# Performance work log

Hardware: AMD Instinct MI355X
Metric: run time of the kernel (lower is better)

## Reference

```python
import jax, jax.numpy as jnp
import numpy as np

B, T, S, H = 8, 512, 512, 128


def setup_inputs() -> dict:
    key = jax.random.key(0)
    ks = jax.random.split(key, 8)
    query = jax.random.normal(ks[0], (B, T, H), dtype=jnp.float32)
    encoder_outputs = jax.random.normal(ks[1], (B, S, H), dtype=jnp.float32)
    src_lengths = jax.random.randint(ks[2], (B,), 1, S + 1)
    src_lengths = src_lengths.at[0].set(S)  # torch mask width == lengths.max() must equal S
    scale = 1.0 / np.sqrt(H)
    W_h = jax.random.normal(ks[3], (H, H), dtype=jnp.float32) * scale
    W_s = jax.random.normal(ks[4], (H, H), dtype=jnp.float32) * scale
    v = jax.random.normal(ks[5], (H,), dtype=jnp.float32) * scale
    W_out_w = jax.random.normal(ks[6], (H, 2 * H), dtype=jnp.float32) * (1.0 / np.sqrt(2 * H))
    W_out_b = jax.random.normal(ks[7], (H,), dtype=jnp.float32) * 0.01
    return {"query": query, "encoder_outputs": encoder_outputs,
            "src_lengths": src_lengths, "W_h": W_h, "W_s": W_s, "v": v,
            "W_out_w": W_out_w, "W_out_b": W_out_b}


def reference(query, encoder_outputs, src_lengths, W_h, W_s, v, W_out_w, W_out_b):
    # query: (B,T,H); encoder_outputs: (B,S,H)
    S_ = encoder_outputs.shape[1]
    WS = jnp.einsum('bth,oh->bto', query, W_s)            # (B,T,H)
    WH = jnp.einsum('bsh,oh->bso', encoder_outputs, W_h)  # (B,S,H)
    # additive scores: v^T tanh(W_s s_t + W_h h_i)  -> (B,T,S)
    scores = jnp.einsum('btsh,h->bts', jnp.tanh(WS[:, :, None, :] + WH[:, None, :, :]), v)
    mask = jnp.arange(S_) < src_lengths[:, None]          # (B,S)
    # faithful quirk: original zeroes (not -inf) masked scores before softmax
    scores = jnp.where(mask[:, None, :], scores, 0.0)
    attn = jax.nn.softmax(scores, axis=-1)                # (B,T,S)
    ct = jnp.einsum('bts,bsh->bth', attn, encoder_outputs)
    concat = jnp.concatenate([ct, query], axis=-1)        # (B,T,2H)
    return jnp.tanh(jnp.einsum('btc,oc->bto', concat, W_out_w) + W_out_b)
```

## Files before the change

### kernel.cpp

```cpp
#include <hip/hip_runtime.h>
#include <hip/hip_fp16.h>

#define NB 8
#define NT 512
#define NS 512
#define NH 128
#define C2LOG2E 2.8853900817779268f

__device__ __forceinline__ float fast_exp2(float x) { return __builtin_amdgcn_exp2f(x); }
__device__ __forceinline__ float fast_rcp(float x)  { return __builtin_amdgcn_rcpf(x); }
__device__ __forceinline__ float fast_tanh(float x) {
  float e = fast_exp2(x * C2LOG2E);
  return 1.0f - 2.0f * fast_rcp(e + 1.0f);
}

__device__ __forceinline__ float dot4(float4 a, float4 b) {
  return (a.x * b.x + a.y * b.y) + (a.z * b.z + a.w * b.w);
}

__device__ __forceinline__ float2 quad_acc2(float4 e, float4 vv,
                                            float2 F0, float2 F1,
                                            float2 F2, float2 F3, float2 acc) {
  float P0x = fmaf(e.x, F0.x, 1.f), P0y = fmaf(e.x, F0.y, 1.f);
  float P1x = fmaf(e.y, F1.x, 1.f), P1y = fmaf(e.y, F1.y, 1.f);
  float P2x = fmaf(e.z, F2.x, 1.f), P2y = fmaf(e.z, F2.y, 1.f);
  float P3x = fmaf(e.w, F3.x, 1.f), P3y = fmaf(e.w, F3.y, 1.f);
  float d01x = P0x * P1x, d01y = P0y * P1y;
  float d23x = P2x * P3x, d23y = P2y * P3y;
  float n01x = fmaf(vv.x, P1x, vv.y * P0x);
  float n01y = fmaf(vv.x, P1y, vv.y * P0y);
  float n23x = fmaf(vv.z, P3x, vv.w * P2x);
  float n23y = fmaf(vv.z, P3y, vv.w * P2y);
  float numx = fmaf(n01x, d23x, n23x * d01x);
  float numy = fmaf(n01y, d23y, n23y * d01y);
  acc.x = fmaf(numx, fast_rcp(d01x * d23x), acc.x);
  acc.y = fmaf(numy, fast_rcp(d01y * d23y), acc.y);
  return acc;
}

__global__ __launch_bounds__(256) void bah_proj_kernel(
    const float* __restrict__ query, const float* __restrict__ enc,
    const float* __restrict__ W_s, const float* __restrict__ W_h,
    const float* __restrict__ Wout, const float* __restrict__ Woutb,
    float* __restrict__ EWS, __half* __restrict__ EWHT,
    __half* __restrict__ ENCW, float* __restrict__ QW2) {
  __shared__ __align__(16) float lds_w[64 * 132];
  __shared__ __align__(16) float lds_x[64 * 132];
  const int set = blockIdx.x >> 7;
  const int blk = blockIdx.x & 127;
  const int rb = blk >> 1, ch = blk & 1;
  const int r0 = rb * 64, c0 = ch * 64;
  const int tid = threadIdx.x;
  const float* in = (set == 1 || set == 2) ? enc : query;
  const float* Wb; int wst;
  if (set == 0)      { Wb = W_s;        wst = 128; }
  else if (set == 1) { Wb = W_h;        wst = 128; }
  else if (set == 2) { Wb = Wout;       wst = 256; }
  else               { Wb = Wout + 128; wst = 256; }
  for (int i = tid; i < 2048; i += 256) {
    int r = i >> 5, c4 = i & 31;
    *(float4*)(lds_w + r * 132 + c4 * 4) =
        *(const float4*)(Wb + (c0 + r) * wst + c4 * 4);
  }
  for (int i = tid; i < 2048; i += 256) {
    int r = i >> 5, c4 = i & 31;
    *(float4*)(lds_x + r * 132 + c4 * 4) =
        *(const float4*)(in + (r0 + r) * NH + c4 * 4);
  }
  __syncthreads();
  const int colg = tid & 15;
  const int rowg = tid >> 4;
  float acc[4][4] = {{0,0,0,0},{0,0,0,0},{0,0,0,0},{0,0,0,0}};
  for (int k4 = 0; k4 < 32; ++k4) {
    float4 xa[4], wb[4];
    #pragma unroll
    for (int i = 0; i < 4; ++i)
      xa[i] = *(const float4*)(lds_x + (rowg * 4 + i) * 132 + k4 * 4);
    #pragma unroll
    for (int m = 0; m < 4; ++m)
      wb[m] = *(const float4*)(lds_w + (colg + 16 * m) * 132 + k4 * 4);
    #pragma unroll
    for (int i = 0; i < 4; ++i)
      #pragma unroll
      for (int m = 0; m < 4; ++m)
        acc[i][m] += dot4(xa[i], wb[m]);
  }
  if (set == 0) {
    #pragma unroll
    for (int i = 0; i < 4; ++i)
      #pragma unroll
      for (int m = 0; m < 4; ++m)
        EWS[(r0 + rowg * 4 + i) * NH + c0 + colg + 16 * m] =
            fast_exp2(C2LOG2E * acc[i][m]);
  } else if (set == 1) {
    __syncthreads();
    #pragma unroll
    for (int i = 0; i < 4; ++i)
      #pragma unroll
      for (int m = 0; m < 4; ++m)
        lds_x[(colg + 16 * m) * 68 + rowg * 4 + i] =
            fminf(fast_exp2(C2LOG2E * acc[i][m]), 60000.f);
    __syncthreads();
    const int b = r0 >> 9, sl0 = r0 & 511;
    const int sc = tid & 15, hb = tid >> 4;
    #pragma unroll
    for (int g = 0; g < 4; ++g) {
      int h = hb + 16 * g;
      float4 f = *(const float4*)(lds_x + h * 68 + sc * 4);
      __half2 p01 = __floats2half2_rn(f.x, f.y);
      __half2 p23 = __floats2half2_rn(f.z, f.w);
      __half2* dst = (__half2*)(EWHT + (size_t)b * NH * NS +
                                (c0 + h) * NS + sl0 + sc * 4);
      dst[0] = p01; dst[1] = p23;
    }
  } else if (set == 2) {
    #pragma unroll
    for (int i = 0; i < 4; ++i)
      #pragma unroll
      for (int m = 0; m < 4; ++m)
        ENCW[(r0 + rowg * 4 + i) * NH + c0 + colg + 16 * m] =
            __float2half_rn(acc[i][m]);
  } else {
    #pragma unroll
    for (int i = 0; i < 4; ++i)
      #pragma unroll
      for (int m = 0; m < 4; ++m) {
        int c = c0 + colg + 16 * m;
        QW2[(r0 + rowg * 4 + i) * NH + c] = acc[i][m] + Woutb[c];
      }
  }
}

__global__ __launch_bounds__(256) void bah_mega_kernel(
    const float* __restrict__ EWS, const __half* __restrict__ EWHT,
    const float* __restrict__ v, const __half* __restrict__ ENCW,
    const float* __restrict__ QW2, const int* __restrict__ src_len,
    float* __restrict__ out) {
  __shared__ __align__(16) float smem[4784];
  float* s_v   = smem;
  float* s_et  = smem + 128;
  float* s_aT  = smem + 656;
  float* s_sc  = smem + 2704;
  float* s_red = smem + 4768;

  const int tid = threadIdx.x;
  const int bb = blockIdx.x >> 7;
  const int t0 = (blockIdx.x & 127) * 4;
  const int len = src_len[bb];

  if (tid < 32) *(float4*)(s_v + tid * 4) = *(const float4*)(v + tid * 4);
  if (tid < 128) {
    int r = tid >> 5, c4 = tid & 31;
    *(float4*)(s_et + r * 132 + c4 * 4) =
        *(const float4*)(EWS + (bb * NT + t0 + r) * NH + c4 * 4);
  }
  __syncthreads();

  float V0;
  {
    float2 vv = *(const float2*)(s_v + (tid & 63) * 2);
    V0 = vv.x + vv.y;
    #pragma unroll
    for (int msk = 1; msk <= 32; msk <<= 1)
      V0 += __shfl_xor(V0, msk, 64);
  }

  const int sbase = tid * 2;
  float2 acc2[4];
  #pragma unroll
  for (int i = 0; i < 4; ++i) { acc2[i].x = 0.f; acc2[i].y = 0.f; }
  const int wave_s0 = (tid & ~63) * 2;
  if (wave_s0 < len) {
    const __half2* fb = (const __half2*)EWHT + (size_t)bb * NH * 256 + tid;
    for (int ho = 0; ho < 16; ++ho) {
      const __half2* fh = fb + ho * 8 * 256;
      float2 F0 = __half22float2(fh[0 * 256]);
      float2 F1 = __half22float2(fh[1 * 256]);
      float2 F2 = __half22float2(fh[2 * 256]);
      float2 F3 = __half22float2(fh[3 * 256]);
      float2 F4 = __half22float2(fh[4 * 256]);
      float2 F5 = __half22float2(fh[5 * 256]);
      float2 F6 = __half22float2(fh[6 * 256]);
      float2 F7 = __half22float2(fh[7 * 256]);
      float4 va = *(const float4*)(s_v + ho * 8);
      float4 vb = *(const float4*)(s_v + ho * 8 + 4);
      #pragma unroll
      for (int tt = 0; tt < 4; ++tt) {
        float4 e0 = *(const float4*)(s_et + tt * 132 + ho * 8);
        float4 e1 = *(const float4*)(s_et + tt * 132 + ho * 8 + 4);
        acc2[tt] = quad_acc2(e0, va, F0, F1, F2, F3, acc2[tt]);
        acc2[tt] = quad_acc2(e1, vb, F4, F5, F6, F7, acc2[tt]);
      }
    }
  }
  #pragma unroll
  for (int tt = 0; tt < 4; ++tt) {
    float2 r;
    r.x = (sbase + 0 < len) ? fmaf(-2.f, acc2[tt].x, V0) : 0.f;
    r.y = (sbase + 1 < len) ? fmaf(-2.f, acc2[tt].y, V0) : 0.f;
    *(float2*)(s_sc + tt * 516 + sbase) = r;
  }
  __syncthreads();

  const int t = tid & 3;
  const int c = tid >> 2;
  const int wv = tid >> 6;
  float pv[8];
  float mx = -3.4e38f;
  #pragma unroll
  for (int k = 0; k < 8; ++k) {
    pv[k] = s_sc[t * 516 + c + 64 * k];
    mx = fmaxf(mx, pv[k]);
  }
  #pragma unroll
  for (int msk = 4; msk <= 32; msk <<= 1)
    mx = fmaxf(mx, __shfl_xor(mx, msk, 64));
  if ((tid & 63) < 4) s_red[wv * 4 + t] = mx;
  __syncthreads();
  #pragma unroll
  for (int j = 0; j < 4; ++j) mx = fmaxf(mx, s_red[j * 4 + t]);
  __syncthreads();
  float sum = 0.f;
  #pragma unroll
  for (int k = 0; k < 8; ++k) {
    pv[k] = fast_exp2((pv[k] - mx) * 1.4426950408889634f);
    sum += pv[k];
  }
  #pragma unroll
  for (int msk = 4; msk <= 32; msk <<= 1)
    sum += __shfl_xor(sum, msk, 64);
  if ((tid & 63) < 4) s_red[wv * 4 + t] = sum;
  __syncthreads();
  sum = 0.f;
  #pragma unroll
  for (int j = 0; j < 4; ++j) sum += s_red[j * 4 + t];
  const float rd = fast_rcp(sum);
  #pragma unroll
  for (int k = 0; k < 8; ++k)
    s_aT[(c + 64 * k) * 4 + t] = pv[k] * rd;
  __syncthreads();

  const int hg = tid & 31, sg = tid >> 5;
  float4 a8[4] = {{0,0,0,0},{0,0,0,0},{0,0,0,0},{0,0,0,0}};
  const __half2* eb = (const __half2*)ENCW + (size_t)bb * NS * 64 + hg * 2;
  for (int k = 0; k < 64; ++k) {
    int s = sg * 64 + k;
    uint2 raw = *(const uint2*)(eb + s * 64);
    float2 f0 = __half22float2(*(const __half2*)&raw.x);
    float2 f1 = __half22float2(*(const __half2*)&raw.y);
    float4 e = {f0.x, f0.y, f1.x, f1.y};
    float4 w = *(const float4*)(s_aT + s * 4);
    a8[0].x += w.x*e.x; a8[0].y += w.x*e.y; a8[0].z += w.x*e.z; a8[0].w += w.x*e.w;
    a8[1].x += w.y*e.x; a8[1].y += w.y*e.y; a8[1].z += w.y*e.z; a8[1].w += w.y*e.w;
    a8[2].x += w.z*e.x; a8[2].y += w.z*e.y; a8[2].z += w.z*e.z; a8[2].w += w.z*e.w;
    a8[3].x += w.w*e.x; a8[3].y += w.w*e.y; a8[3].z += w.w*e.z; a8[3].w += w.w*e.w;
  }
  #pragma unroll
  for (int i = 0; i < 4; ++i) {
    a8[i].x += __shfl_xor(a8[i].x, 32, 64);
    a8[i].y += __shfl_xor(a8[i].y, 32, 64);
    a8[i].z += __shfl_xor(a8[i].z, 32, 64);
    a8[i].w += __shfl_xor(a8[i].w, 32, 64);
  }
  float* lred = s_sc;
  if ((tid & 63) < 32) {
    #pragma unroll
    for (int i = 0; i < 4; ++i)
      *(float4*)(lred + wv * 512 + i * 128 + hg * 4) = a8[i];
  }
  __syncthreads();
  {
    int tt = tid >> 6, h2 = tid & 63;
    float2 o = {0.f, 0.f};
    #pragma unroll
    for (int j = 0; j < 4; ++j) {
      float2 p = *(const float2*)(lred + j * 512 + tt * 128 + h2 * 2);
      o.x += p.x; o.y += p.y;
    }
    const int row = bb * NT + t0 + tt;
    float2 q2 = *(const float2*)(QW2 + row * NH + h2 * 2);
    float2 r;
    r.x = fast_tanh(o.x + q2.x);
    r.y = fast_tanh(o.y + q2.y);
    *(float2*)(out + row * NH + h2 * 2) = r;
  }
}

extern "C" void kernel_launch(void* const* d_in, const int* in_sizes, int n_in,
                              void* d_out, int out_size, void* d_ws, size_t ws_size,
                              hipStream_t stream) {
  const float* query = (const float*)d_in[0];
  const float* enc   = (const float*)d_in[1];
  const int*   slen  = (const int*)d_in[2];
  const float* W_h   = (const float*)d_in[3];
  const float* W_s   = (const float*)d_in[4];
  const float* v     = (const float*)d_in[5];
  const float* Woutw = (const float*)d_in[6];
  const float* Woutb = (const float*)d_in[7];
  float* out = (float*)d_out;

  float* ws = (float*)d_ws;
  float*  EWS  = ws;
  float*  QW2  = ws + 524288;
  __half* EWHT = (__half*)(ws + 1048576);
  __half* ENCW = (__half*)(ws + 1310720);

  bah_proj_kernel<<<512, 256, 0, stream>>>(query, enc, W_s, W_h, Woutw,
                                           Woutb, EWS, EWHT, ENCW, QW2);
  bah_mega_kernel<<<1024, 256, 0, stream>>>(EWS, EWHT, v, ENCW, QW2, slen, out);
}
```

Before: 120.1 us.

## Halve queries per block in attention kernel and stage ENCW stores through LDS

The main attention kernel now handles 2 query rows per block instead of 4 and launches twice as many blocks. This shrinks the per-block shared-memory and register footprint and adds a launch bound hinting 8 blocks per CU, aiming for higher occupancy. The trade-off is that each block re-reads the EWHT and ENCW tiles for half as many queries, which doubles that global/L2 traffic. Separately, the projection kernel's ENCW fp16 output is staged through LDS so each thread writes 16-byte vector stores instead of scattered 2-byte stores.

```diff
diff --git a/kernel.cpp b/kernel.cpp
--- a/kernel.cpp
+++ b/kernel.cpp
@@ -114,12 +114,22 @@
       dst[0] = p01; dst[1] = p23;
     }
   } else if (set == 2) {
+    __syncthreads();
     #pragma unroll
     for (int i = 0; i < 4; ++i)
       #pragma unroll
       for (int m = 0; m < 4; ++m)
-        ENCW[(r0 + rowg * 4 + i) * NH + c0 + colg + 16 * m] =
-            __float2half_rn(acc[i][m]);
+        lds_w[(rowg * 4 + i) * 68 + colg + 16 * m] = acc[i][m];
+    __syncthreads();
+    const int rr = tid >> 2, cb = (tid & 3) * 16;
+    const float* src = lds_w + rr * 68 + cb;
+    __half2 h[8];
+    #pragma unroll
+    for (int q = 0; q < 8; ++q)
+      h[q] = __floats2half2_rn(src[2 * q], src[2 * q + 1]);
+    uint4* dst = (uint4*)(ENCW + (size_t)(r0 + rr) * NH + c0 + cb);
+    dst[0] = ((uint4*)h)[0];
+    dst[1] = ((uint4*)h)[1];
   } else {
     #pragma unroll
     for (int i = 0; i < 4; ++i)
@@ -131,25 +141,25 @@
   }
 }
 
-__global__ __launch_bounds__(256) void bah_mega_kernel(
+__global__ __launch_bounds__(256, 8) void bah_mega_kernel(
     const float* __restrict__ EWS, const __half* __restrict__ EWHT,
     const float* __restrict__ v, const __half* __restrict__ ENCW,
     const float* __restrict__ QW2, const int* __restrict__ src_len,
     float* __restrict__ out) {
-  __shared__ __align__(16) float smem[4784];
+  __shared__ __align__(16) float smem[2456];
   float* s_v   = smem;
   float* s_et  = smem + 128;
-  float* s_aT  = smem + 656;
-  float* s_sc  = smem + 2704;
-  float* s_red = smem + 4768;
+  float* s_aT  = smem + 392;
+  float* s_sc  = smem + 1416;
+  float* s_red = smem + 2448;
 
   const int tid = threadIdx.x;
-  const int bb = blockIdx.x >> 7;
-  const int t0 = (blockIdx.x & 127) * 4;
+  const int bb = blockIdx.x >> 8;
+  const int t0 = (blockIdx.x & 255) * 2;
   const int len = src_len[bb];
 
   if (tid < 32) *(float4*)(s_v + tid * 4) = *(const float4*)(v + tid * 4);
-  if (tid < 128) {
+  if (tid < 64) {
     int r = tid >> 5, c4 = tid & 31;
     *(float4*)(s_et + r * 132 + c4 * 4) =
         *(const float4*)(EWS + (bb * NT + t0 + r) * NH + c4 * 4);
@@ -166,9 +176,8 @@
   }
 
   const int sbase = tid * 2;
-  float2 acc2[4];
-  #pragma unroll
-  for (int i = 0; i < 4; ++i) { acc2[i].x = 0.f; acc2[i].y = 0.f; }
+  float2 acc2[2];
+  acc2[0].x = 0.f; acc2[0].y = 0.f; acc2[1].x = 0.f; acc2[1].y = 0.f;
   const int wave_s0 = (tid & ~63) * 2;
   if (wave_s0 < len) {
     const __half2* fb = (const __half2*)EWHT + (size_t)bb * NH * 256 + tid;
@@ -185,7 +194,7 @@
       float4 va = *(const float4*)(s_v + ho * 8);
       float4 vb = *(const float4*)(s_v + ho * 8 + 4);
       #pragma unroll
-      for (int tt = 0; tt < 4; ++tt) {
+      for (int tt = 0; tt < 2; ++tt) {
         float4 e0 = *(const float4*)(s_et + tt * 132 + ho * 8);
         float4 e1 = *(const float4*)(s_et + tt * 132 + ho * 8 + 4);
         acc2[tt] = quad_acc2(e0, va, F0, F1, F2, F3, acc2[tt]);
@@ -194,7 +203,7 @@
     }
   }
   #pragma unroll
-  for (int tt = 0; tt < 4; ++tt) {
+  for (int tt = 0; tt < 2; ++tt) {
     float2 r;
     r.x = (sbase + 0 < len) ? fmaf(-2.f, acc2[tt].x, V0) : 0.f;
     r.y = (sbase + 1 < len) ? fmaf(-2.f, acc2[tt].y, V0) : 0.f;
@@ -202,87 +211,78 @@
   }
   __syncthreads();
 
-  const int t = tid & 3;
-  const int c = tid >> 2;
+  const int t = tid & 1;
+  const int c = tid >> 1;
   const int wv = tid >> 6;
-  float pv[8];
+  float pv[4];
   float mx = -3.4e38f;
   #pragma unroll
-  for (int k = 0; k < 8; ++k) {
-    pv[k] = s_sc[t * 516 + c + 64 * k];
+  for (int k = 0; k < 4; ++k) {
+    pv[k] = s_sc[t * 516 + c + 128 * k];
     mx = fmaxf(mx, pv[k]);
   }
   #pragma unroll
-  for (int msk = 4; msk <= 32; msk <<= 1)
+  for (int msk = 2; msk <= 32; msk <<= 1)
     mx = fmaxf(mx, __shfl_xor(mx, msk, 64));
-  if ((tid & 63) < 4) s_red[wv * 4 + t] = mx;
-  __syncthreads();
-  #pragma unroll
-  for (int j = 0; j < 4; ++j) mx = fmaxf(mx, s_red[j * 4 + t]);
+  if ((tid & 63) < 2) s_red[wv * 2 + t] = mx;
+  __syncthreads();
+  #pragma unroll
+  for (int j = 0; j < 4; ++j) mx = fmaxf(mx, s_red[j * 2 + t]);
   __syncthreads();
   float sum = 0.f;
   #pragma unroll
-  for (int k = 0; k < 8; ++k) {
+  for (int k = 0; k < 4; ++k) {
     pv[k] = fast_exp2((pv[k] - mx) * 1.4426950408889634f);
     sum += pv[k];
   }
   #pragma unroll
-  for (int msk = 4; msk <= 32; msk <<= 1)
+  for (int msk = 2; msk <= 32; msk <<= 1)
     sum += __shfl_xor(sum, msk, 64);
-  if ((tid & 63) < 4) s_red[wv * 4 + t] = sum;
+  if ((tid & 63) < 2) s_red[wv * 2 + t] = sum;
   __syncthreads();
   sum = 0.f;
   #pragma unroll
-  for (int j = 0; j < 4; ++j) sum += s_red[j * 4 + t];
+  for (int j = 0; j < 4; ++j) sum += s_red[j * 2 + t];
   const float rd = fast_rcp(sum);
   #pragma unroll
-  for (int k = 0; k < 8; ++k)
-    s_aT[(c + 64 * k) * 4 + t] = pv[k] * rd;
+  for (int k = 0; k < 4; ++k)
+    s_aT[(c + 128 * k) * 2 + t] = pv[k] * rd;
   __syncthreads();
 
   const int hg = tid & 31, sg = tid >> 5;
-  float4 a8[4] = {{0,0,0,0},{0,0,0,0},{0,0,0,0},{0,0,0,0}};
+  float4 a0 = {0,0,0,0}, a1 = {0,0,0,0};
   const __half2* eb = (const __half2*)ENCW + (size_t)bb * NS * 64 + hg * 2;
   for (int k = 0; k < 64; ++k) {
     int s = sg * 64 + k;
     uint2 raw = *(const uint2*)(eb + s * 64);
     float2 f0 = __half22float2(*(const __half2*)&raw.x);
     float2 f1 = __half22float2(*(const __half2*)&raw.y);
-    float4 e = {f0.x, f0.y, f1.x, f1.y};
-    float4 w = *(const float4*)(s_aT + s * 4);
-    a8[0].x += w.x*e.x; a8[0].y += w.x*e.y; a8[0].z += w.x*e.z; a8[0].w += w.x*e.w;
-    a8[1].x += w.y*e.x; a8[1].y += w.y*e.y; a8[1].z += w.y*e.z; a8[1].w += w.y*e.w;
-    a8[2].x += w.z*e.x; a8[2].y += w.z*e.y; a8[2].z += w.z*e.z; a8[2].w += w.z*e.w;
-    a8[3].x += w.w*e.x; a8[3].y += w.w*e.y; a8[3].z += w.w*e.z; a8[3].w += w.w*e.w;
-  }
-  #pragma unroll
-  for (int i = 0; i < 4; ++i) {
-    a8[i].x += __shfl_xor(a8[i].x, 32, 64);
-    a8[i].y += __shfl_xor(a8[i].y, 32, 64);
-    a8[i].z += __shfl_xor(a8[i].z, 32, 64);
-    a8[i].w += __shfl_xor(a8[i].w, 32, 64);
-  }
+    float2 w = *(const float2*)(s_aT + s * 2);
+    a0.x += w.x*f0.x; a0.y += w.x*f0.y; a0.z += w.x*f1.x; a0.w += w.x*f1.y;
+    a1.x += w.y*f0.x; a1.y += w.y*f0.y; a1.z += w.y*f1.x; a1.w += w.y*f1.y;
+  }
+  a0.x += __shfl_xor(a0.x, 32, 64);
+  a0.y += __shfl_xor(a0.y, 32, 64);
+  a0.z += __shfl_xor(a0.z, 32, 64);
+  a0.w += __shfl_xor(a0.w, 32, 64);
+  a1.x += __shfl_xor(a1.x, 32, 64);
+  a1.y += __shfl_xor(a1.y, 32, 64);
+  a1.z += __shfl_xor(a1.z, 32, 64);
+  a1.w += __shfl_xor(a1.w, 32, 64);
   float* lred = s_sc;
   if ((tid & 63) < 32) {
-    #pragma unroll
-    for (int i = 0; i < 4; ++i)
-      *(float4*)(lred + wv * 512 + i * 128 + hg * 4) = a8[i];
+    *(float4*)(lred + wv * 256 + hg * 4) = a0;
+    *(float4*)(lred + wv * 256 + 128 + hg * 4) = a1;
   }
   __syncthreads();
   {
-    int tt = tid >> 6, h2 = tid & 63;
-    float2 o = {0.f, 0.f};
-    #pragma unroll
-    for (int j = 0; j < 4; ++j) {
-      float2 p = *(const float2*)(lred + j * 512 + tt * 128 + h2 * 2);
-      o.x += p.x; o.y += p.y;
-    }
+    int tt = tid >> 7, hh = tid & 127;
+    float o = 0.f;
+    #pragma unroll
+    for (int j = 0; j < 4; ++j)
+      o += lred[j * 256 + tt * 128 + hh];
     const int row = bb * NT + t0 + tt;
-    float2 q2 = *(const float2*)(QW2 + row * NH + h2 * 2);
-    float2 r;
-    r.x = fast_tanh(o.x + q2.x);
-    r.y = fast_tanh(o.y + q2.y);
-    *(float2*)(out + row * NH + h2 * 2) = r;
+    out[row * NH + hh] = fast_tanh(o + QW2[row * NH + hh]);
   }
 }
 
@@ -307,5 +307,5 @@
 
   bah_proj_kernel<<<512, 256, 0, stream>>>(query, enc, W_s, W_h, Woutw,
                                            Woutb, EWS, EWHT, ENCW, QW2);
-  bah_mega_kernel<<<1024, 256, 0, stream>>>(EWS, EWHT, v, ENCW, QW2, slen, out);
-}
+  bah_mega_kernel<<<2048, 256, 0, stream>>>(EWS, EWHT, v, ENCW, QW2, slen, out);
+}
```

New measurement: 119.9 us. About the same (-0.1%).

## Split mega kernel into score and context kernels via half-precision attention buffer

Applied to the files above, without the earlier changes.

Splits the fused score+context kernel in two. The score kernel writes transposed softmax weights as fp16 to a workspace buffer. A separate context kernel with 512 threads then handles 8 query rows per block, so each ENCW element loaded is reused across more rows. The ENCW store in the projection kernel is also staged through LDS so it can be written with wide vector stores. The trade is an extra launch, an extra global round trip for the attention matrix, and fp16 rounding of the attention weights.

```diff
diff --git a/kernel.cpp b/kernel.cpp
--- a/kernel.cpp
+++ b/kernel.cpp
@@ -114,12 +114,22 @@
       dst[0] = p01; dst[1] = p23;
     }
   } else if (set == 2) {
+    __syncthreads();
     #pragma unroll
     for (int i = 0; i < 4; ++i)
       #pragma unroll
       for (int m = 0; m < 4; ++m)
-        ENCW[(r0 + rowg * 4 + i) * NH + c0 + colg + 16 * m] =
-            __float2half_rn(acc[i][m]);
+        lds_w[(rowg * 4 + i) * 68 + colg + 16 * m] = acc[i][m];
+    __syncthreads();
+    const int rr = tid >> 2, cb = (tid & 3) * 16;
+    const float* src = lds_w + rr * 68 + cb;
+    __half2 h[8];
+    #pragma unroll
+    for (int q = 0; q < 8; ++q)
+      h[q] = __floats2half2_rn(src[2 * q], src[2 * q + 1]);
+    uint4* dst = (uint4*)(ENCW + (size_t)(r0 + rr) * NH + c0 + cb);
+    dst[0] = ((uint4*)h)[0];
+    dst[1] = ((uint4*)h)[1];
   } else {
     #pragma unroll
     for (int i = 0; i < 4; ++i)
@@ -131,17 +141,15 @@
   }
 }
 
-__global__ __launch_bounds__(256) void bah_mega_kernel(
+__global__ __launch_bounds__(256) void bah_score_kernel(
     const float* __restrict__ EWS, const __half* __restrict__ EWHT,
-    const float* __restrict__ v, const __half* __restrict__ ENCW,
-    const float* __restrict__ QW2, const int* __restrict__ src_len,
-    float* __restrict__ out) {
-  __shared__ __align__(16) float smem[4784];
+    const float* __restrict__ v, const int* __restrict__ src_len,
+    __half* __restrict__ aT) {
+  __shared__ __align__(16) float smem[2736];
   float* s_v   = smem;
   float* s_et  = smem + 128;
-  float* s_aT  = smem + 656;
-  float* s_sc  = smem + 2704;
-  float* s_red = smem + 4768;
+  float* s_sc  = smem + 656;
+  float* s_red = smem + 2720;
 
   const int tid = threadIdx.x;
   const int bb = blockIdx.x >> 7;
@@ -235,54 +243,74 @@
   #pragma unroll
   for (int j = 0; j < 4; ++j) sum += s_red[j * 4 + t];
   const float rd = fast_rcp(sum);
+  __half* ab = aT + (size_t)bb * NS * NT + t0 + t;
   #pragma unroll
   for (int k = 0; k < 8; ++k)
-    s_aT[(c + 64 * k) * 4 + t] = pv[k] * rd;
-  __syncthreads();
-
+    ab[(size_t)(c + 64 * k) * NT] = __float2half_rn(pv[k] * rd);
+}
+
+__global__ __launch_bounds__(512) void bah_ct_kernel(
+    const __half* __restrict__ aT, const __half* __restrict__ ENCW,
+    const float* __restrict__ QW2, float* __restrict__ out) {
+  __shared__ __align__(16) float lred[8192];
+  const int tid = threadIdx.x;
+  const int bb = blockIdx.x >> 6;
+  const int t0 = (blockIdx.x & 63) * 8;
   const int hg = tid & 31, sg = tid >> 5;
-  float4 a8[4] = {{0,0,0,0},{0,0,0,0},{0,0,0,0},{0,0,0,0}};
+  const int wv = tid >> 6;
+
+  float4 a8[8] = {{0,0,0,0},{0,0,0,0},{0,0,0,0},{0,0,0,0},
+                  {0,0,0,0},{0,0,0,0},{0,0,0,0},{0,0,0,0}};
   const __half2* eb = (const __half2*)ENCW + (size_t)bb * NS * 64 + hg * 2;
-  for (int k = 0; k < 64; ++k) {
-    int s = sg * 64 + k;
-    uint2 raw = *(const uint2*)(eb + s * 64);
+  const __half* wb = aT + (size_t)bb * NS * NT + t0;
+  for (int k = 0; k < 32; ++k) {
+    int s = sg * 32 + k;
+    uint2 raw = *(const uint2*)(eb + (size_t)s * 64);
     float2 f0 = __half22float2(*(const __half2*)&raw.x);
     float2 f1 = __half22float2(*(const __half2*)&raw.y);
     float4 e = {f0.x, f0.y, f1.x, f1.y};
-    float4 w = *(const float4*)(s_aT + s * 4);
-    a8[0].x += w.x*e.x; a8[0].y += w.x*e.y; a8[0].z += w.x*e.z; a8[0].w += w.x*e.w;
-    a8[1].x += w.y*e.x; a8[1].y += w.y*e.y; a8[1].z += w.y*e.z; a8[1].w += w.y*e.w;
-    a8[2].x += w.z*e.x; a8[2].y += w.z*e.y; a8[2].z += w.z*e.z; a8[2].w += w.z*e.w;
-    a8[3].x += w.w*e.x; a8[3].y += w.w*e.y; a8[3].z += w.w*e.z; a8[3].w += w.w*e.w;
-  }
-  #pragma unroll
-  for (int i = 0; i < 4; ++i) {
+    uint4 wraw = *(const uint4*)(wb + (size_t)s * NT);
+    const __half2* wh = (const __half2*)&wraw;
+    float2 w01 = __half22float2(wh[0]);
+    float2 w23 = __half22float2(wh[1]);
+    float2 w45 = __half22float2(wh[2]);
+    float2 w67 = __half22float2(wh[3]);
+    float w[8] = {w01.x, w01.y, w23.x, w23.y, w45.x, w45.y, w67.x, w67.y};
+    #pragma unroll
+    for (int i = 0; i < 8; ++i) {
+      a8[i].x += w[i] * e.x; a8[i].y += w[i] * e.y;
+      a8[i].z += w[i] * e.z; a8[i].w += w[i] * e.w;
+    }
+  }
+  #pragma unroll
+  for (int i = 0; i < 8; ++i) {
     a8[i].x += __shfl_xor(a8[i].x, 32, 64);
     a8[i].y += __shfl_xor(a8[i].y, 32, 64);
     a8[i].z += __shfl_xor(a8[i].z, 32, 64);
     a8[i].w += __shfl_xor(a8[i].w, 32, 64);
   }
-  float* lred = s_sc;
   if ((tid & 63) < 32) {
     #pragma unroll
-    for (int i = 0; i < 4; ++i)
-      *(float4*)(lred + wv * 512 + i * 128 + hg * 4) = a8[i];
-  }
-  __syncthreads();
-  {
-    int tt = tid >> 6, h2 = tid & 63;
-    float2 o = {0.f, 0.f};
-    #pragma unroll
-    for (int j = 0; j < 4; ++j) {
-      float2 p = *(const float2*)(lred + j * 512 + tt * 128 + h2 * 2);
-      o.x += p.x; o.y += p.y;
+    for (int i = 0; i < 8; ++i)
+      *(float4*)(lred + wv * 1024 + i * 128 + hg * 4) = a8[i];
+  }
+  __syncthreads();
+  if (tid < 256) {
+    int tt = tid >> 5, hh = tid & 31;
+    float4 o = {0.f, 0.f, 0.f, 0.f};
+    #pragma unroll
+    for (int j = 0; j < 8; ++j) {
+      float4 p = *(const float4*)(lred + j * 1024 + tt * 128 + hh * 4);
+      o.x += p.x; o.y += p.y; o.z += p.z; o.w += p.w;
     }
     const int row = bb * NT + t0 + tt;
-    float2 q2 = *(const float2*)(QW2 + row * NH + h2 * 2);
-    float2 r;
-    r.x = fast_tanh(o.x + q2.x);
-    r.y = fast_tanh(o.y + q2.y);
-    *(float2*)(out + row * NH + h2 * 2) = r;
+    float4 q4 = *(const float4*)(QW2 + row * NH + hh * 4);
+    float4 r;
+    r.x = fast_tanh(o.x + q4.x);
+    r.y = fast_tanh(o.y + q4.y);
+    r.z = fast_tanh(o.z + q4.z);
+    r.w = fast_tanh(o.w + q4.w);
+    *(float4*)(out + row * NH + hh * 4) = r;
   }
 }
 
@@ -304,8 +332,10 @@
   float*  QW2  = ws + 524288;
   __half* EWHT = (__half*)(ws + 1048576);
   __half* ENCW = (__half*)(ws + 1310720);
+  __half* aT   = (__half*)(ws + 1572864);
 
   bah_proj_kernel<<<512, 256, 0, stream>>>(query, enc, W_s, W_h, Woutw,
                                            Woutb, EWS, EWHT, ENCW, QW2);
-  bah_mega_kernel<<<1024, 256, 0, stream>>>(EWS, EWHT, v, ENCW, QW2, slen, out);
-}
+  bah_score_kernel<<<1024, 256, 0, stream>>>(EWS, EWHT, v, slen, aT);
+  bah_ct_kernel<<<512, 512, 0, stream>>>(aT, ENCW, QW2, out);
+}
```

Result: slower. 123.4 us (+2.8%).

## Prefetch global loads one iteration ahead and coalesce ENCW stores via LDS

Applied to the files above, without the earlier changes.

The score loop now loads the next group of eight EWHT half2 values into registers while computing on the current group, and the context loop prefetches the next ENCW row the same way. Both are meant to hide global-load latency behind FMA work. The ENCW write in the projection kernel is staged through LDS so each thread stores two 16-byte vectors instead of scattered 2-byte halves. This adds register pressure and extra barriers, which may reduce occupancy.

```diff
diff --git a/kernel.cpp b/kernel.cpp
--- a/kernel.cpp
+++ b/kernel.cpp
@@ -114,12 +114,22 @@
       dst[0] = p01; dst[1] = p23;
     }
   } else if (set == 2) {
+    __syncthreads();
     #pragma unroll
     for (int i = 0; i < 4; ++i)
       #pragma unroll
       for (int m = 0; m < 4; ++m)
-        ENCW[(r0 + rowg * 4 + i) * NH + c0 + colg + 16 * m] =
-            __float2half_rn(acc[i][m]);
+        lds_w[(rowg * 4 + i) * 68 + colg + 16 * m] = acc[i][m];
+    __syncthreads();
+    const int rr = tid >> 2, cb = (tid & 3) * 16;
+    const float* src = lds_w + rr * 68 + cb;
+    __half2 h[8];
+    #pragma unroll
+    for (int q = 0; q < 8; ++q)
+      h[q] = __floats2half2_rn(src[2 * q], src[2 * q + 1]);
+    uint4* dst = (uint4*)(ENCW + (size_t)(r0 + rr) * NH + c0 + cb);
+    dst[0] = ((uint4*)h)[0];
+    dst[1] = ((uint4*)h)[1];
   } else {
     #pragma unroll
     for (int i = 0; i < 4; ++i)
@@ -172,16 +182,24 @@
   const int wave_s0 = (tid & ~63) * 2;
   if (wave_s0 < len) {
     const __half2* fb = (const __half2*)EWHT + (size_t)bb * NH * 256 + tid;
+    __half2 F[8];
+    #pragma unroll
+    for (int j = 0; j < 8; ++j) F[j] = fb[j * 256];
     for (int ho = 0; ho < 16; ++ho) {
-      const __half2* fh = fb + ho * 8 * 256;
-      float2 F0 = __half22float2(fh[0 * 256]);
-      float2 F1 = __half22float2(fh[1 * 256]);
-      float2 F2 = __half22float2(fh[2 * 256]);
-      float2 F3 = __half22float2(fh[3 * 256]);
-      float2 F4 = __half22float2(fh[4 * 256]);
-      float2 F5 = __half22float2(fh[5 * 256]);
-      float2 F6 = __half22float2(fh[6 * 256]);
-      float2 F7 = __half22float2(fh[7 * 256]);
+      __half2 Fn[8];
+      if (ho < 15) {
+        const __half2* fh = fb + (ho + 1) * 8 * 256;
+        #pragma unroll
+        for (int j = 0; j < 8; ++j) Fn[j] = fh[j * 256];
+      }
+      float2 F0 = __half22float2(F[0]);
+      float2 F1 = __half22float2(F[1]);
+      float2 F2 = __half22float2(F[2]);
+      float2 F3 = __half22float2(F[3]);
+      float2 F4 = __half22float2(F[4]);
+      float2 F5 = __half22float2(F[5]);
+      float2 F6 = __half22float2(F[6]);
+      float2 F7 = __half22float2(F[7]);
       float4 va = *(const float4*)(s_v + ho * 8);
       float4 vb = *(const float4*)(s_v + ho * 8 + 4);
       #pragma unroll
@@ -191,6 +209,8 @@
         acc2[tt] = quad_acc2(e0, va, F0, F1, F2, F3, acc2[tt]);
         acc2[tt] = quad_acc2(e1, vb, F4, F5, F6, F7, acc2[tt]);
       }
+      #pragma unroll
+      for (int j = 0; j < 8; ++j) F[j] = Fn[j];
     }
   }
   #pragma unroll
@@ -243,9 +263,11 @@
   const int hg = tid & 31, sg = tid >> 5;
   float4 a8[4] = {{0,0,0,0},{0,0,0,0},{0,0,0,0},{0,0,0,0}};
   const __half2* eb = (const __half2*)ENCW + (size_t)bb * NS * 64 + hg * 2;
+  uint2 raw = *(const uint2*)(eb + (size_t)(sg * 64) * 64);
   for (int k = 0; k < 64; ++k) {
     int s = sg * 64 + k;
-    uint2 raw = *(const uint2*)(eb + s * 64);
+    uint2 nraw;
+    if (k < 63) nraw = *(const uint2*)(eb + (size_t)(s + 1) * 64);
     float2 f0 = __half22float2(*(const __half2*)&raw.x);
     float2 f1 = __half22float2(*(const __half2*)&raw.y);
     float4 e = {f0.x, f0.y, f1.x, f1.y};
@@ -254,6 +276,7 @@
     a8[1].x += w.y*e.x; a8[1].y += w.y*e.y; a8[1].z += w.y*e.z; a8[1].w += w.y*e.w;
     a8[2].x += w.z*e.x; a8[2].y += w.z*e.y; a8[2].z += w.z*e.z; a8[2].w += w.z*e.w;
     a8[3].x += w.w*e.x; a8[3].y += w.w*e.y; a8[3].z += w.w*e.z; a8[3].w += w.w*e.w;
+    raw = nraw;
   }
   #pragma unroll
   for (int i = 0; i < 4; ++i) {
```

New measurement: 120.9 us. No clear change (+0.7%).
